# Kernel optimization log

Hardware: AMD Instinct MI355X
Metric: run time of the kernel (lower is better)

## Reference

```python
import jax, jax.numpy as jnp
import numpy as np

B, IN_CH, N, DIM, PH, HID, K = 4, 128, 2048, 256, 64, 1024, 16
EPS = 1e-5


def conv1(x, w, b):
    # 1x1 Conv1d: x (B,C,N), w (O,C) -> (B,O,N)
    return jnp.einsum('oc,bcn->bon', w, x) + b[None, :, None]


def conv2(x, w, b):
    # 1x1 Conv2d: x (B,C,N,K), w (O,C) -> (B,O,N,K)
    return jnp.einsum('oc,bcnk->bonk', w, x) + b[None, :, None, None]


def bn2(x, g, beta, mean, var):
    # eval-mode BatchNorm2d over channel dim of (B,C,N,K)
    scale = g * jax.lax.rsqrt(var + EPS)
    return x * scale[None, :, None, None] + (beta - mean * scale)[None, :, None, None]


def query_knn(pos, k):
    # pos: (B,3,N). Returns (B,N,K) indices of k nearest neighbors (incl. self).
    p = jnp.transpose(pos, (0, 2, 1))                     # (B,N,3)
    sq = jnp.sum(p * p, axis=-1)                          # (B,N)
    dist = sq[:, :, None] + sq[:, None, :] - 2.0 * jnp.einsum('bnc,bmc->bnm', p, p)
    _, idx = jax.lax.top_k(-dist, k)                      # smallest distances first
    return idx


def group(feat, idx):
    # feat: (B,C,N), idx: (B,N,K) -> (B,C,N,K) where out[b,c,i,k]=feat[b,c,idx[b,i,k]]
    b, c, n = feat.shape
    k = idx.shape[-1]
    ib = jnp.broadcast_to(idx.reshape(b, 1, n * k), (b, c, n * k))
    return jnp.take_along_axis(feat, ib, axis=2).reshape(b, c, n, k)


def setup_inputs() -> dict:
    key = jax.random.key(0)
    ks = jax.random.split(key, 12)
    s = 0.02
    return {
        'x': jax.random.normal(ks[0], (B, IN_CH, N), jnp.float32),
        'pos': jax.random.normal(ks[1], (B, 3, N), jnp.float32),
        'ls_w': jax.random.normal(ks[2], (DIM, IN_CH), jnp.float32) * s,
        'ls_b': jnp.zeros((DIM,), jnp.float32),
        'kw': jax.random.normal(ks[3], (DIM, DIM), jnp.float32) * s,
        'kb': jnp.zeros((DIM,), jnp.float32),
        'qw': jax.random.normal(ks[4], (DIM, DIM), jnp.float32) * s,
        'qb': jnp.zeros((DIM,), jnp.float32),
        'vw': jax.random.normal(ks[5], (DIM, DIM), jnp.float32) * s,
        'vb': jnp.zeros((DIM,), jnp.float32),
        'pw1': jax.random.normal(ks[6], (PH, 3), jnp.float32) * s,
        'pb1': jnp.zeros((PH,), jnp.float32),
        'pg': jnp.ones((PH,), jnp.float32),
        'pbeta': jnp.zeros((PH,), jnp.float32),
        'pmean': jnp.zeros((PH,), jnp.float32),
        'pvar': jnp.ones((PH,), jnp.float32),
        'pw2': jax.random.normal(ks[7], (DIM, PH), jnp.float32) * s,
        'pb2': jnp.zeros((DIM,), jnp.float32),
        'aw1': jax.random.normal(ks[8], (HID, DIM), jnp.float32) * s,
        'ab1': jnp.zeros((HID,), jnp.float32),
        'ag': jnp.ones((HID,), jnp.float32),
        'abeta': jnp.zeros((HID,), jnp.float32),
        'amean': jnp.zeros((HID,), jnp.float32),
        'avar': jnp.ones((HID,), jnp.float32),
        'aw2': jax.random.normal(ks[9], (DIM, HID), jnp.float32) * s,
        'ab2': jnp.zeros((DIM,), jnp.float32),
        'lw': jax.random.normal(ks[10], (IN_CH, DIM), jnp.float32) * s,
        'lb': jnp.zeros((IN_CH,), jnp.float32),
    }


def reference(x, pos, ls_w, ls_b, kw, kb, qw, qb, vw, vb,
              pw1, pb1, pg, pbeta, pmean, pvar, pw2, pb2,
              aw1, ab1, ag, abeta, amean, avar, aw2, ab2, lw, lb):
    identity = x
    h = conv1(x, ls_w, ls_b)                              # (B,DIM,N)
    idx = query_knn(pos, K)                               # (B,N,K) int32
    key_f = group(conv1(h, kw, kb), idx)                  # (B,DIM,N,K)
    value = conv1(h, vw, vb)                              # (B,DIM,N)
    query = conv1(h, qw, qb)                              # (B,DIM,N)
    qk_rel = query[:, :, :, None] - key_f                 # (B,DIM,N,K)
    pos_rel = pos[:, :, :, None] - group(pos, idx)        # (B,3,N,K)
    pe = conv2(jax.nn.relu(bn2(conv2(pos_rel, pw1, pb1), pg, pbeta, pmean, pvar)), pw2, pb2)
    attn = conv2(jax.nn.relu(bn2(conv2(qk_rel + pe, aw1, ab1), ag, abeta, amean, avar)), aw2, ab2)
    attn = jax.nn.softmax(attn, axis=-1)                  # softmax over K
    val_g = group(value, idx) + pe                        # (B,DIM,N,K)
    agg = jnp.sum(attn * val_g, axis=-1)                  # (B,DIM,N)
    y = conv1(agg, lw, lb)                                # (B,IN_CH,N)
    return y + identity
```

## Files before the change

### kernel.cpp

```cpp
#include <hip/hip_runtime.h>
#include <hip/hip_bf16.h>
#include <math.h>

#define B_    4
#define CIN   128
#define NPTS  2048
#define DIM   256
#define PH    64
#define HIDN  1024
#define KNN_  16
#define BN    (B_*NPTS)
#define CC    (BN*KNN_)
#define QKV   768
#define EPS_  1e-5f

typedef __bf16 bf16;
typedef __bf16 bf16x8 __attribute__((ext_vector_type(8)));
typedef __bf16 bf16x4 __attribute__((ext_vector_type(4)));
typedef float  f32x4  __attribute__((ext_vector_type(4)));

__global__ __launch_bounds__(256) void prep_kernel(
    const float* __restrict__ ls_w, const float* __restrict__ qw,
    const float* __restrict__ kw,   const float* __restrict__ vw,
    const float* __restrict__ pw2,  const float* __restrict__ aw1,
    const float* __restrict__ aw2,  const float* __restrict__ lw,
    const float* __restrict__ qb,   const float* __restrict__ kb,
    const float* __restrict__ vb,
    const float* __restrict__ pb1,  const float* __restrict__ pg,
    const float* __restrict__ pbeta,const float* __restrict__ pmean,
    const float* __restrict__ pvar,
    const float* __restrict__ ab1,  const float* __restrict__ ag,
    const float* __restrict__ abeta,const float* __restrict__ amean,
    const float* __restrict__ avar,
    bf16* ls_wb, bf16* wqkvb, bf16* pw2b, bf16* aw1b, bf16* aw2b, bf16* lwb,
    float* pe_scale, float* pe_shift, float* at_scale, float* at_shift,
    float* bqkv)
{
  long e = (long)blockIdx.x * 256 + threadIdx.x;
  if (e < 32768)  { ls_wb[e] = (bf16)ls_w[e]; return; } e -= 32768;
  if (e < 196608) {
    int row = (int)(e >> 8), col = (int)(e & 255);
    float v = (row < 256) ? qw[row * 256 + col]
            : (row < 512) ? kw[(row - 256) * 256 + col]
                          : vw[(row - 512) * 256 + col];
    wqkvb[e] = (bf16)v; return;
  } e -= 196608;
  if (e < 16384)  { pw2b[e] = (bf16)pw2[e];  return; } e -= 16384;
  if (e < 262144) { aw1b[e] = (bf16)aw1[e];  return; } e -= 262144;
  if (e < 262144) { aw2b[e] = (bf16)aw2[e];  return; } e -= 262144;
  if (e < 32768)  { lwb[e]  = (bf16)lw[e];   return; } e -= 32768;
  if (e < 64) {
    float sc = pg[e] * rsqrtf(pvar[e] + EPS_);
    pe_scale[e] = sc;
    pe_shift[e] = sc * pb1[e] + pbeta[e] - pmean[e] * sc;
    return;
  } e -= 64;
  if (e < 1024) {
    float sc = ag[e] * rsqrtf(avar[e] + EPS_);
    at_scale[e] = sc;
    at_shift[e] = sc * ab1[e] + abeta[e] - amean[e] * sc;
    return;
  } e -= 1024;
  if (e < 768) {
    bqkv[e] = (e < 256) ? qb[e] : (e < 512) ? kb[e - 256] : vb[e - 512];
  }
}

__global__ __launch_bounds__(256) void transpose_x_kernel(
    const float* __restrict__ x, bf16* __restrict__ xT)
{
  long e = (long)blockIdx.x * 256 + threadIdx.x;
  int ch = (int)(e & (CIN - 1));
  long i = e >> 7;
  int n = (int)(i & (NPTS - 1));
  int b = (int)(i >> 11);
  xT[e] = (bf16)x[((long)b * CIN + ch) * NPTS + n];
}

__global__ __launch_bounds__(256) void knn_kernel(
    const float* __restrict__ pos, int* __restrict__ idx_out)
{
  __shared__ float px[NPTS], py[NPTS], pz[NPTS];
  const int tid = threadIdx.x;
  const int lane = tid & 63, wave = tid >> 6;
  const int q = blockIdx.x * 4 + wave;
  const int b = q >> 11;
  const int n = q & (NPTS - 1);
  const float* p = pos + (long)b * 3 * NPTS;
  for (int j = tid; j < NPTS; j += 256) {
    px[j] = p[j]; py[j] = p[NPTS + j]; pz[j] = p[2 * NPTS + j];
  }
  __syncthreads();
  float qx = px[n], qy = py[n], qz = pz[n];
  float qs = qx * qx + qy * qy + qz * qz;
  float d[32];
#pragma unroll
  for (int j = 0; j < 32; ++j) {
    int pt = j * 64 + lane;
    float x = px[pt], y = py[pt], z = pz[pt];
    float s2 = x * x + y * y + z * z;
    float dt = qx * x + qy * y + qz * z;
    d[j] = qs + s2 - 2.f * dt;
  }
  for (int r = 0; r < KNN_; ++r) {
    float bv = 1e30f; int bj = 0;
#pragma unroll
    for (int j = 0; j < 32; ++j)
      if (d[j] < bv) { bv = d[j]; bj = j; }
    int bi = bj * 64 + lane;
#pragma unroll
    for (int off = 32; off >= 1; off >>= 1) {
      float ov = __shfl_xor(bv, off);
      int   oi = __shfl_xor(bi, off);
      if (ov < bv || (ov == bv && oi < bi)) { bv = ov; bi = oi; }
    }
    if (lane == 0) idx_out[(long)q * KNN_ + r] = bi;
#pragma unroll
    for (int j = 0; j < 32; ++j)
      if (bi == j * 64 + lane) d[j] = 1e30f;
  }
}

template<int KD, bool OBF16>
__global__ __launch_bounds__(256) void gemmT_kernel(
    const bf16* __restrict__ inT, const bf16* __restrict__ Wb,
    const float* __restrict__ bias, void* __restrict__ outp, int O)
{
  const int tid = threadIdx.x;
  const int lane = tid & 63, wave = tid >> 6;
  const int row16 = lane & 15, grp = lane >> 4;
  const long i0 = (long)blockIdx.x * 64 + (wave & 1) * 32;
  const long o0 = (long)blockIdx.y * 64 + (wave >> 1) * 32;
  f32x4 acc[2][2] = {};
  const bf16* a0p = inT + (i0 + row16) * KD + grp * 8;
  const bf16* a1p = a0p + 16 * KD;
  const bf16* b0p = Wb + (o0 + row16) * KD + grp * 8;
  const bf16* b1p = b0p + 16 * KD;
#pragma unroll
  for (int ks = 0; ks < KD / 32; ++ks) {
    bf16x8 a0 = *(const bf16x8*)(a0p + ks * 32);
    bf16x8 a1 = *(const bf16x8*)(a1p + ks * 32);
    bf16x8 b0 = *(const bf16x8*)(b0p + ks * 32);
    bf16x8 b1 = *(const bf16x8*)(b1p + ks * 32);
    acc[0][0] = __builtin_amdgcn_mfma_f32_16x16x32_bf16(a0, b0, acc[0][0], 0, 0, 0);
    acc[0][1] = __builtin_amdgcn_mfma_f32_16x16x32_bf16(a0, b1, acc[0][1], 0, 0, 0);
    acc[1][0] = __builtin_amdgcn_mfma_f32_16x16x32_bf16(a1, b0, acc[1][0], 0, 0, 0);
    acc[1][1] = __builtin_amdgcn_mfma_f32_16x16x32_bf16(a1, b1, acc[1][1], 0, 0, 0);
  }
#pragma unroll
  for (int ot = 0; ot < 2; ++ot) {
    long o = o0 + ot * 16 + row16;
    float bv = bias[o];
#pragma unroll
    for (int it = 0; it < 2; ++it) {
#pragma unroll
      for (int r = 0; r < 4; ++r) {
        long i = i0 + it * 16 + grp * 4 + r;
        float v = acc[it][ot][r] + bv;
        if (OBF16) ((bf16*)outp)[i * O + o] = (bf16)v;
        else       ((float*)outp)[i * O + o] = v;
      }
    }
  }
}

__global__ __launch_bounds__(256, 3) void attn_fused_kernel(
    const bf16* __restrict__ qkvT, const float* __restrict__ pos,
    const int* __restrict__ idx, const float* __restrict__ pw1,
    const float* __restrict__ pe_scale, const float* __restrict__ pe_shift,
    const bf16* __restrict__ pw2b, const float* __restrict__ pb2,
    const bf16* __restrict__ aw1b, const bf16* __restrict__ aw2b,
    const float* __restrict__ at_scale, const float* __restrict__ at_shift,
    const float* __restrict__ ab2, bf16* __restrict__ aggT)
{
  __shared__ __align__(16) bf16 u_lds[64][264];
  __shared__ __align__(16) bf16 tbuf[64 * 136];
  __shared__ float rel_lds[64][4];
  __shared__ int   idx_lds[64];
  bf16 (*t_lds)[136]  = (bf16(*)[136])tbuf;
  bf16 (*hid_lds)[72] = (bf16(*)[72])tbuf;

  const int tid = threadIdx.x;
  const int lane = tid & 63, wave = tid >> 6;
  const int row16 = lane & 15, grp = lane >> 4;
  const long c0 = (long)blockIdx.x * 64;
  const int bn0 = blockIdx.x * 4;
  const int b = bn0 >> 11;
  const float* pB = pos + (long)b * 3 * NPTS;
  const int os = wave * 64;
  const int hs = wave * 32;

  if (tid < 64) {
    int nb = idx[c0 + tid];
    idx_lds[tid] = nb;
    int n = (bn0 + (tid >> 4)) & (NPTS - 1);
    rel_lds[tid][0] = pB[n] - pB[nb];
    rel_lds[tid][1] = pB[NPTS + n] - pB[NPTS + nb];
    rel_lds[tid][2] = pB[2 * NPTS + n] - pB[2 * NPTS + nb];
  }
  __syncthreads();

  {
    int c = tid & 63, jq = tid >> 6;
    float rx = rel_lds[c][0], ry = rel_lds[c][1], rz = rel_lds[c][2];
#pragma unroll
    for (int jj = 0; jj < 16; ++jj) {
      int j = jq * 16 + jj;
      float v = pw1[j * 3] * rx + pw1[j * 3 + 1] * ry + pw1[j * 3 + 2] * rz;
      v = pe_scale[j] * v + pe_shift[j];
      hid_lds[c][j] = (bf16)fmaxf(v, 0.f);
    }
  }
  __syncthreads();

  f32x4 accpe[4][4] = {};
  f32x4 accpeT[4][4] = {};
#pragma unroll
  for (int ks = 0; ks < 2; ++ks) {
    bf16x8 ah[4], bw[4];
#pragma unroll
    for (int ct = 0; ct < 4; ++ct)
      ah[ct] = *(const bf16x8*)&hid_lds[ct * 16 + row16][ks * 32 + grp * 8];
#pragma unroll
    for (int ot = 0; ot < 4; ++ot)
      bw[ot] = *(const bf16x8*)(pw2b + (long)(os + ot * 16 + row16) * PH + ks * 32 + grp * 8);
#pragma unroll
    for (int ct = 0; ct < 4; ++ct)
#pragma unroll
      for (int ot = 0; ot < 4; ++ot) {
        accpe[ct][ot]  = __builtin_amdgcn_mfma_f32_16x16x32_bf16(ah[ct], bw[ot], accpe[ct][ot], 0, 0, 0);
        accpeT[ct][ot] = __builtin_amdgcn_mfma_f32_16x16x32_bf16(bw[ot], ah[ct], accpeT[ct][ot], 0, 0, 0);
      }
  }

  bf16x4 pe_bf[4][4];
#pragma unroll
  for (int ot = 0; ot < 4; ++ot) {
    float pb2v = pb2[os + ot * 16 + row16];
#pragma unroll
    for (int ct = 0; ct < 4; ++ct)
#pragma unroll
      for (int r = 0; r < 4; ++r)
        pe_bf[ct][ot][r] = (bf16)(accpe[ct][ot][r] + pb2v);
  }

#pragma unroll
  for (int ct = 0; ct < 4; ++ct) {
    int nb = idx_lds[ct * 16 + row16];
    const bf16* krow = qkvT + ((long)b * NPTS + nb) * QKV + 256 + os;
    const bf16* qrow = qkvT + (long)(bn0 + ct) * QKV + os;
#pragma unroll
    for (int ot = 0; ot < 4; ++ot) {
      int o4 = ot * 16 + grp * 4;
      bf16x4 k4 = *(const bf16x4*)(krow + o4);
      bf16x4 q4 = *(const bf16x4*)(qrow + o4);
      f32x4 pb4 = *(const f32x4*)&pb2[os + o4];
      bf16x4 u4;
#pragma unroll
      for (int r = 0; r < 4; ++r)
        u4[r] = (bf16)((float)q4[r] - (float)k4[r] + accpeT[ct][ot][r] + pb4[r]);
      *(bf16x4*)&u_lds[ct * 16 + row16][os + o4] = u4;
    }
  }
  __syncthreads();

  f32x4 acc2[4][4] = {};
  for (int jc = 0; jc < 8; ++jc) {
    const int hg = jc * 128 + hs;
    f32x4 acc1[4][2] = {};
#pragma unroll
    for (int ks = 0; ks < 8; ++ks) {
      bf16x8 bu[4], aw[2];
#pragma unroll
      for (int ct = 0; ct < 4; ++ct)
        bu[ct] = *(const bf16x8*)&u_lds[ct * 16 + row16][ks * 32 + grp * 8];
#pragma unroll
      for (int jt = 0; jt < 2; ++jt)
        aw[jt] = *(const bf16x8*)(aw1b + (long)(hg + jt * 16 + row16) * DIM + ks * 32 + grp * 8);
#pragma unroll
      for (int ct = 0; ct < 4; ++ct)
#pragma unroll
        for (int jt = 0; jt < 2; ++jt)
          acc1[ct][jt] = __builtin_amdgcn_mfma_f32_16x16x32_bf16(aw[jt], bu[ct], acc1[ct][jt], 0, 0, 0);
    }
#pragma unroll
    for (int jt = 0; jt < 2; ++jt) {
      int jb = hg + jt * 16 + grp * 4;
      f32x4 sc4 = *(const f32x4*)&at_scale[jb];
      f32x4 sh4 = *(const f32x4*)&at_shift[jb];
#pragma unroll
      for (int ct = 0; ct < 4; ++ct) {
        bf16x4 pk;
#pragma unroll
        for (int r = 0; r < 4; ++r) {
          float v = sc4[r] * acc1[ct][jt][r] + sh4[r];
          pk[r] = (bf16)fmaxf(v, 0.f);
        }
        *(bf16x4*)&t_lds[ct * 16 + row16][hs + jt * 16 + grp * 4] = pk;
      }
    }
    __syncthreads();
#pragma unroll
    for (int ks2 = 0; ks2 < 4; ++ks2) {
      bf16x8 a2[4], b2;
#pragma unroll
      for (int ct = 0; ct < 4; ++ct)
        a2[ct] = *(const bf16x8*)&t_lds[ct * 16 + row16][ks2 * 32 + grp * 8];
#pragma unroll
      for (int ot = 0; ot < 4; ++ot) {
        b2 = *(const bf16x8*)(aw2b + (long)(os + ot * 16 + row16) * HIDN + jc * 128 + ks2 * 32 + grp * 8);
#pragma unroll
        for (int ct = 0; ct < 4; ++ct)
          acc2[ct][ot] = __builtin_amdgcn_mfma_f32_16x16x32_bf16(a2[ct], b2, acc2[ct][ot], 0, 0, 0);
      }
    }
    __syncthreads();
  }

#pragma unroll
  for (int ct = 0; ct < 4; ++ct) {
#pragma unroll
    for (int ot = 0; ot < 4; ++ot) {
      int o = os + ot * 16 + row16;
      float ab = ab2[o];
      float l[4];
      float m = -1e30f;
#pragma unroll
      for (int r = 0; r < 4; ++r) {
        l[r] = acc2[ct][ot][r] + ab;
        m = fmaxf(m, l[r]);
      }
      m = fmaxf(m, __shfl_xor(m, 16));
      m = fmaxf(m, __shfl_xor(m, 32));
      float s = 0.f;
#pragma unroll
      for (int r = 0; r < 4; ++r) { l[r] = expf(l[r] - m); s += l[r]; }
      s += __shfl_xor(s, 16);
      s += __shfl_xor(s, 32);
      float inv = 1.f / s;
      float agg = 0.f;
#pragma unroll
      for (int r = 0; r < 4; ++r) {
        int c = ct * 16 + grp * 4 + r;
        int nb = idx_lds[c];
        float vv = (float)qkvT[((long)b * NPTS + nb) * QKV + 512 + o];
        agg += l[r] * (vv + (float)pe_bf[ct][ot][r]);
      }
      agg *= inv;
      agg += __shfl_xor(agg, 16);
      agg += __shfl_xor(agg, 32);
      if (grp == 0) aggT[(long)(bn0 + ct) * DIM + o] = (bf16)agg;
    }
  }
}

__global__ __launch_bounds__(256) void final_kernel(
    const bf16* __restrict__ aggT, const bf16* __restrict__ lwb,
    const float* __restrict__ lb, const float* __restrict__ x,
    float* __restrict__ out)
{
  const int tid = threadIdx.x;
  const int lane = tid & 63, wave = tid >> 6;
  const int row16 = lane & 15, grp = lane >> 4;
  const long i0 = (long)blockIdx.x * 64 + (wave & 1) * 32;
  const int o0 = blockIdx.y * 64 + (wave >> 1) * 32;
  f32x4 acc[2][2] = {};
  const bf16* a0p = aggT + (i0 + row16) * DIM + grp * 8;
  const bf16* a1p = a0p + 16 * DIM;
  const bf16* b0p = lwb + (long)(o0 + row16) * DIM + grp * 8;
  const bf16* b1p = b0p + 16 * DIM;
#pragma unroll
  for (int ks = 0; ks < 8; ++ks) {
    bf16x8 a0 = *(const bf16x8*)(a0p + ks * 32);
    bf16x8 a1 = *(const bf16x8*)(a1p + ks * 32);
    bf16x8 b0 = *(const bf16x8*)(b0p + ks * 32);
    bf16x8 b1 = *(const bf16x8*)(b1p + ks * 32);
    acc[0][0] = __builtin_amdgcn_mfma_f32_16x16x32_bf16(a0, b0, acc[0][0], 0, 0, 0);
    acc[0][1] = __builtin_amdgcn_mfma_f32_16x16x32_bf16(a0, b1, acc[0][1], 0, 0, 0);
    acc[1][0] = __builtin_amdgcn_mfma_f32_16x16x32_bf16(a1, b0, acc[1][0], 0, 0, 0);
    acc[1][1] = __builtin_amdgcn_mfma_f32_16x16x32_bf16(a1, b1, acc[1][1], 0, 0, 0);
  }
#pragma unroll
  for (int ot = 0; ot < 2; ++ot) {
    int o = o0 + ot * 16 + row16;
    float bv = lb[o];
#pragma unroll
    for (int it = 0; it < 2; ++it) {
#pragma unroll
      for (int r = 0; r < 4; ++r) {
        long i = i0 + it * 16 + grp * 4 + r;
        int bb = (int)(i >> 11);
        int n = (int)(i & (NPTS - 1));
        long off = ((long)bb * CIN + o) * NPTS + n;
        out[off] = acc[it][ot][r] + bv + x[off];
      }
    }
  }
}

extern "C" void kernel_launch(void* const* d_in, const int* in_sizes, int n_in,
                              void* d_out, int out_size, void* d_ws, size_t ws_size,
                              hipStream_t stream)
{
  const float* x     = (const float*)d_in[0];
  const float* pos   = (const float*)d_in[1];
  const float* ls_w  = (const float*)d_in[2];
  const float* ls_b  = (const float*)d_in[3];
  const float* kw    = (const float*)d_in[4];
  const float* kb    = (const float*)d_in[5];
  const float* qw    = (const float*)d_in[6];
  const float* qb    = (const float*)d_in[7];
  const float* vw    = (const float*)d_in[8];
  const float* vb    = (const float*)d_in[9];
  const float* pw1   = (const float*)d_in[10];
  const float* pb1   = (const float*)d_in[11];
  const float* pg    = (const float*)d_in[12];
  const float* pbeta = (const float*)d_in[13];
  const float* pmean = (const float*)d_in[14];
  const float* pvar  = (const float*)d_in[15];
  const float* pw2   = (const float*)d_in[16];
  const float* pb2   = (const float*)d_in[17];
  const float* aw1   = (const float*)d_in[18];
  const float* ab1   = (const float*)d_in[19];
  const float* ag    = (const float*)d_in[20];
  const float* abeta = (const float*)d_in[21];
  const float* amean = (const float*)d_in[22];
  const float* avar  = (const float*)d_in[23];
  const float* aw2   = (const float*)d_in[24];
  const float* ab2   = (const float*)d_in[25];
  const float* lw    = (const float*)d_in[26];
  const float* lb    = (const float*)d_in[27];

  char* ws = (char*)d_ws;
  size_t off = 0;
  auto alloc = [&](size_t bytes) -> void* {
    void* p = ws + off;
    off = (off + bytes + 255) & ~(size_t)255;
    return p;
  };

  bf16* ls_wb = (bf16*)alloc(32768 * 2);
  bf16* wqkvb = (bf16*)alloc(196608 * 2);
  bf16* pw2b  = (bf16*)alloc(16384 * 2);
  bf16* aw1b  = (bf16*)alloc(262144 * 2);
  bf16* aw2b  = (bf16*)alloc(262144 * 2);
  bf16* lwb   = (bf16*)alloc(32768 * 2);
  float* pe_scale = (float*)alloc(64 * 4);
  float* pe_shift = (float*)alloc(64 * 4);
  float* at_scale = (float*)alloc(1024 * 4);
  float* at_shift = (float*)alloc(1024 * 4);
  float* bqkv = (float*)alloc(768 * 4);
  int*  idx  = (int*)alloc((size_t)CC * 4);
  bf16* xT   = (bf16*)alloc((size_t)BN * CIN * 2);
  bf16* hT   = (bf16*)alloc((size_t)BN * DIM * 2);
  bf16* qkvT = (bf16*)alloc((size_t)BN * QKV * 2);
  bf16* aggT = (bf16*)alloc((size_t)BN * DIM * 2);

  prep_kernel<<<dim3((804672 + 255) / 256), 256, 0, stream>>>(
      ls_w, qw, kw, vw, pw2, aw1, aw2, lw, qb, kb, vb,
      pb1, pg, pbeta, pmean, pvar, ab1, ag, abeta, amean, avar,
      ls_wb, wqkvb, pw2b, aw1b, aw2b, lwb,
      pe_scale, pe_shift, at_scale, at_shift, bqkv);

  transpose_x_kernel<<<dim3(BN * CIN / 256), 256, 0, stream>>>(x, xT);

  knn_kernel<<<dim3(BN / 4), 256, 0, stream>>>(pos, idx);

  gemmT_kernel<128, true><<<dim3(BN / 64, DIM / 64), 256, 0, stream>>>(xT, ls_wb, ls_b, hT, DIM);

  gemmT_kernel<256, true><<<dim3(BN / 64, QKV / 64), 256, 0, stream>>>(hT, wqkvb, bqkv, qkvT, QKV);

  attn_fused_kernel<<<dim3(CC / 64), 256, 0, stream>>>(
      qkvT, pos, idx, pw1, pe_scale, pe_shift, pw2b, pb2,
      aw1b, aw2b, at_scale, at_shift, ab2, aggT);

  final_kernel<<<dim3(BN / 64, CIN / 64), 256, 0, stream>>>(aggT, lwb, lb, x, (float*)d_out);
}
```

Measured before the change: 533.7 us.

## Split QKV buffers and restructure attention kernel to cut register pressure

The QKV projection now writes separate q, k and v arrays with a 256-element row stride, so the neighbour gathers in the attention kernel touch compact rows instead of 768-wide interleaved ones. Inside the fused attention kernel, the transposed positional-encoding accumulator is computed per column tile right before use rather than held for all tiles, and the first hidden GEMM accumulates one j-tile at a time. Both changes shrink live accumulator registers, which matters under the 3-blocks-per-CU launch bound. The u_lds row padding also changes to alter the LDS bank pattern. In exchange, u_lds fragments are reloaded once per j-tile, and there is an extra select on the output pointer in the QKV epilogue.

```diff
diff --git a/kernel.cpp b/kernel.cpp
--- a/kernel.cpp
+++ b/kernel.cpp
@@ -164,8 +164,53 @@
   }
 }
 
+__global__ __launch_bounds__(256) void gemmT_qkv_kernel(
+    const bf16* __restrict__ inT, const bf16* __restrict__ Wb,
+    const float* __restrict__ bias,
+    bf16* __restrict__ qTb, bf16* __restrict__ kTb, bf16* __restrict__ vTb)
+{
+  const int tid = threadIdx.x;
+  const int lane = tid & 63, wave = tid >> 6;
+  const int row16 = lane & 15, grp = lane >> 4;
+  const long i0 = (long)blockIdx.x * 64 + (wave & 1) * 32;
+  const long o0 = (long)blockIdx.y * 64 + (wave >> 1) * 32;
+  f32x4 acc[2][2] = {};
+  const bf16* a0p = inT + (i0 + row16) * DIM + grp * 8;
+  const bf16* a1p = a0p + 16 * DIM;
+  const bf16* b0p = Wb + (o0 + row16) * DIM + grp * 8;
+  const bf16* b1p = b0p + 16 * DIM;
+#pragma unroll
+  for (int ks = 0; ks < 8; ++ks) {
+    bf16x8 a0 = *(const bf16x8*)(a0p + ks * 32);
+    bf16x8 a1 = *(const bf16x8*)(a1p + ks * 32);
+    bf16x8 b0 = *(const bf16x8*)(b0p + ks * 32);
+    bf16x8 b1 = *(const bf16x8*)(b1p + ks * 32);
+    acc[0][0] = __builtin_amdgcn_mfma_f32_16x16x32_bf16(a0, b0, acc[0][0], 0, 0, 0);
+    acc[0][1] = __builtin_amdgcn_mfma_f32_16x16x32_bf16(a0, b1, acc[0][1], 0, 0, 0);
+    acc[1][0] = __builtin_amdgcn_mfma_f32_16x16x32_bf16(a1, b0, acc[1][0], 0, 0, 0);
+    acc[1][1] = __builtin_amdgcn_mfma_f32_16x16x32_bf16(a1, b1, acc[1][1], 0, 0, 0);
+  }
+#pragma unroll
+  for (int ot = 0; ot < 2; ++ot) {
+    long o = o0 + ot * 16 + row16;
+    int third = (int)(o >> 8);
+    bf16* outp = third == 0 ? qTb : third == 1 ? kTb : vTb;
+    int oo = (int)(o & 255);
+    float bv = bias[o];
+#pragma unroll
+    for (int it = 0; it < 2; ++it) {
+#pragma unroll
+      for (int r = 0; r < 4; ++r) {
+        long i = i0 + it * 16 + grp * 4 + r;
+        outp[i * DIM + oo] = (bf16)(acc[it][ot][r] + bv);
+      }
+    }
+  }
+}
+
 __global__ __launch_bounds__(256, 3) void attn_fused_kernel(
-    const bf16* __restrict__ qkvT, const float* __restrict__ pos,
+    const bf16* __restrict__ qTb, const bf16* __restrict__ kTb,
+    const bf16* __restrict__ vTb, const float* __restrict__ pos,
     const int* __restrict__ idx, const float* __restrict__ pw1,
     const float* __restrict__ pe_scale, const float* __restrict__ pe_shift,
     const bf16* __restrict__ pw2b, const float* __restrict__ pb2,
@@ -173,7 +218,7 @@
     const float* __restrict__ at_scale, const float* __restrict__ at_shift,
     const float* __restrict__ ab2, bf16* __restrict__ aggT)
 {
-  __shared__ __align__(16) bf16 u_lds[64][264];
+  __shared__ __align__(16) bf16 u_lds[64][272];
   __shared__ __align__(16) bf16 tbuf[64 * 136];
   __shared__ float rel_lds[64][4];
   __shared__ int   idx_lds[64];
@@ -213,42 +258,52 @@
   }
   __syncthreads();
 
-  f32x4 accpe[4][4] = {};
-  f32x4 accpeT[4][4] = {};
-#pragma unroll
-  for (int ks = 0; ks < 2; ++ks) {
-    bf16x8 ah[4], bw[4];
-#pragma unroll
-    for (int ct = 0; ct < 4; ++ct)
-      ah[ct] = *(const bf16x8*)&hid_lds[ct * 16 + row16][ks * 32 + grp * 8];
+  bf16x8 bw[2][4];
+#pragma unroll
+  for (int ks = 0; ks < 2; ++ks)
 #pragma unroll
     for (int ot = 0; ot < 4; ++ot)
-      bw[ot] = *(const bf16x8*)(pw2b + (long)(os + ot * 16 + row16) * PH + ks * 32 + grp * 8);
-#pragma unroll
-    for (int ct = 0; ct < 4; ++ct)
-#pragma unroll
-      for (int ot = 0; ot < 4; ++ot) {
-        accpe[ct][ot]  = __builtin_amdgcn_mfma_f32_16x16x32_bf16(ah[ct], bw[ot], accpe[ct][ot], 0, 0, 0);
-        accpeT[ct][ot] = __builtin_amdgcn_mfma_f32_16x16x32_bf16(bw[ot], ah[ct], accpeT[ct][ot], 0, 0, 0);
-      }
-  }
+      bw[ks][ot] = *(const bf16x8*)(pw2b + (long)(os + ot * 16 + row16) * PH + ks * 32 + grp * 8);
 
   bf16x4 pe_bf[4][4];
-#pragma unroll
-  for (int ot = 0; ot < 4; ++ot) {
-    float pb2v = pb2[os + ot * 16 + row16];
-#pragma unroll
-    for (int ct = 0; ct < 4; ++ct)
-#pragma unroll
-      for (int r = 0; r < 4; ++r)
-        pe_bf[ct][ot][r] = (bf16)(accpe[ct][ot][r] + pb2v);
+  {
+    f32x4 accpe[4][4] = {};
+#pragma unroll
+    for (int ks = 0; ks < 2; ++ks) {
+      bf16x8 ah[4];
+#pragma unroll
+      for (int ct = 0; ct < 4; ++ct)
+        ah[ct] = *(const bf16x8*)&hid_lds[ct * 16 + row16][ks * 32 + grp * 8];
+#pragma unroll
+      for (int ct = 0; ct < 4; ++ct)
+#pragma unroll
+        for (int ot = 0; ot < 4; ++ot)
+          accpe[ct][ot] = __builtin_amdgcn_mfma_f32_16x16x32_bf16(ah[ct], bw[ks][ot], accpe[ct][ot], 0, 0, 0);
+    }
+#pragma unroll
+    for (int ot = 0; ot < 4; ++ot) {
+      float pb2v = pb2[os + ot * 16 + row16];
+#pragma unroll
+      for (int ct = 0; ct < 4; ++ct)
+#pragma unroll
+        for (int r = 0; r < 4; ++r)
+          pe_bf[ct][ot][r] = (bf16)(accpe[ct][ot][r] + pb2v);
+    }
   }
 
 #pragma unroll
   for (int ct = 0; ct < 4; ++ct) {
+    f32x4 aT[4] = {};
+#pragma unroll
+    for (int ks = 0; ks < 2; ++ks) {
+      bf16x8 ah = *(const bf16x8*)&hid_lds[ct * 16 + row16][ks * 32 + grp * 8];
+#pragma unroll
+      for (int ot = 0; ot < 4; ++ot)
+        aT[ot] = __builtin_amdgcn_mfma_f32_16x16x32_bf16(bw[ks][ot], ah, aT[ot], 0, 0, 0);
+    }
     int nb = idx_lds[ct * 16 + row16];
-    const bf16* krow = qkvT + ((long)b * NPTS + nb) * QKV + 256 + os;
-    const bf16* qrow = qkvT + (long)(bn0 + ct) * QKV + os;
+    const bf16* krow = kTb + ((long)b * NPTS + nb) * DIM + os;
+    const bf16* qrow = qTb + (long)(bn0 + ct) * DIM + os;
 #pragma unroll
     for (int ot = 0; ot < 4; ++ot) {
       int o4 = ot * 16 + grp * 4;
@@ -258,7 +313,7 @@
       bf16x4 u4;
 #pragma unroll
       for (int r = 0; r < 4; ++r)
-        u4[r] = (bf16)((float)q4[r] - (float)k4[r] + accpeT[ct][ot][r] + pb4[r]);
+        u4[r] = (bf16)((float)q4[r] - (float)k4[r] + aT[ot][r] + pb4[r]);
       *(bf16x4*)&u_lds[ct * 16 + row16][os + o4] = u4;
     }
   }
@@ -267,24 +322,18 @@
   f32x4 acc2[4][4] = {};
   for (int jc = 0; jc < 8; ++jc) {
     const int hg = jc * 128 + hs;
-    f32x4 acc1[4][2] = {};
-#pragma unroll
-    for (int ks = 0; ks < 8; ++ks) {
-      bf16x8 bu[4], aw[2];
-#pragma unroll
-      for (int ct = 0; ct < 4; ++ct)
-        bu[ct] = *(const bf16x8*)&u_lds[ct * 16 + row16][ks * 32 + grp * 8];
-#pragma unroll
-      for (int jt = 0; jt < 2; ++jt)
-        aw[jt] = *(const bf16x8*)(aw1b + (long)(hg + jt * 16 + row16) * DIM + ks * 32 + grp * 8);
-#pragma unroll
-      for (int ct = 0; ct < 4; ++ct)
-#pragma unroll
-        for (int jt = 0; jt < 2; ++jt)
-          acc1[ct][jt] = __builtin_amdgcn_mfma_f32_16x16x32_bf16(aw[jt], bu[ct], acc1[ct][jt], 0, 0, 0);
-    }
 #pragma unroll
     for (int jt = 0; jt < 2; ++jt) {
+      f32x4 acc1[4] = {};
+#pragma unroll
+      for (int ks = 0; ks < 8; ++ks) {
+        bf16x8 aw = *(const bf16x8*)(aw1b + (long)(hg + jt * 16 + row16) * DIM + ks * 32 + grp * 8);
+#pragma unroll
+        for (int ct = 0; ct < 4; ++ct) {
+          bf16x8 bu = *(const bf16x8*)&u_lds[ct * 16 + row16][ks * 32 + grp * 8];
+          acc1[ct] = __builtin_amdgcn_mfma_f32_16x16x32_bf16(aw, bu, acc1[ct], 0, 0, 0);
+        }
+      }
       int jb = hg + jt * 16 + grp * 4;
       f32x4 sc4 = *(const f32x4*)&at_scale[jb];
       f32x4 sh4 = *(const f32x4*)&at_shift[jb];
@@ -293,7 +342,7 @@
         bf16x4 pk;
 #pragma unroll
         for (int r = 0; r < 4; ++r) {
-          float v = sc4[r] * acc1[ct][jt][r] + sh4[r];
+          float v = sc4[r] * acc1[ct][r] + sh4[r];
           pk[r] = (bf16)fmaxf(v, 0.f);
         }
         *(bf16x4*)&t_lds[ct * 16 + row16][hs + jt * 16 + grp * 4] = pk;
@@ -343,7 +392,7 @@
       for (int r = 0; r < 4; ++r) {
         int c = ct * 16 + grp * 4 + r;
         int nb = idx_lds[c];
-        float vv = (float)qkvT[((long)b * NPTS + nb) * QKV + 512 + o];
+        float vv = (float)vTb[((long)b * NPTS + nb) * DIM + o];
         agg += l[r] * (vv + (float)pe_bf[ct][ot][r]);
       }
       agg *= inv;
@@ -453,7 +502,9 @@
   int*  idx  = (int*)alloc((size_t)CC * 4);
   bf16* xT   = (bf16*)alloc((size_t)BN * CIN * 2);
   bf16* hT   = (bf16*)alloc((size_t)BN * DIM * 2);
-  bf16* qkvT = (bf16*)alloc((size_t)BN * QKV * 2);
+  bf16* qTb  = (bf16*)alloc((size_t)BN * DIM * 2);
+  bf16* kTb  = (bf16*)alloc((size_t)BN * DIM * 2);
+  bf16* vTb  = (bf16*)alloc((size_t)BN * DIM * 2);
   bf16* aggT = (bf16*)alloc((size_t)BN * DIM * 2);
 
   prep_kernel<<<dim3((804672 + 255) / 256), 256, 0, stream>>>(
@@ -468,10 +519,10 @@
 
   gemmT_kernel<128, true><<<dim3(BN / 64, DIM / 64), 256, 0, stream>>>(xT, ls_wb, ls_b, hT, DIM);
 
-  gemmT_kernel<256, true><<<dim3(BN / 64, QKV / 64), 256, 0, stream>>>(hT, wqkvb, bqkv, qkvT, QKV);
+  gemmT_qkv_kernel<<<dim3(BN / 64, QKV / 64), 256, 0, stream>>>(hT, wqkvb, bqkv, qTb, kTb, vTb);
 
   attn_fused_kernel<<<dim3(CC / 64), 256, 0, stream>>>(
-      qkvT, pos, idx, pw1, pe_scale, pe_shift, pw2b, pb2,
+      qTb, kTb, vTb, pos, idx, pw1, pe_scale, pe_shift, pw2b, pb2,
       aw1b, aw2b, at_scale, at_shift, ab2, aggT);
 
   final_kernel<<<dim3(BN / 64, CIN / 64), 256, 0, stream>>>(aggT, lwb, lb, x, (float*)d_out);
```

After: 546.8 us. +2.5%, slower.
